# Kernel optimization log

Measured on AMD Instinct MI355X. Metric: run time of the kernel, lower is better.

Reference implementation:

```python
import jax, jax.numpy as jnp
import numpy as np

ANCHORS = np.array([[116.0, 90.0], [156.0, 198.0], [373.0, 326.0]], dtype=np.float32)
IMAGE_SIZE = 2048.0
IGNORE_THRES = 0.5
OBJ_SCALE = 100.0
NO_OBJ_SCALE = 1.0
EPS = 1e-16
BCE_EPS = 1e-12


def _wh_iou(anchors, gwh):
    # anchors: [A,2], gwh: [T,2] -> iou [A,T]
    aw, ah = anchors[:, 0:1], anchors[:, 1:2]            # [A,1]
    gw, gh = gwh[None, :, 0], gwh[None, :, 1]            # [1,T]
    inter = jnp.minimum(aw, gw) * jnp.minimum(ah, gh)
    union = aw * ah + gw * gh - inter
    return inter / (union + EPS)


def _bbox_iou_xywh(box1, box2):
    # boxes [T,4] in (cx, cy, w, h)
    b1x1, b1x2 = box1[:, 0] - box1[:, 2] / 2, box1[:, 0] + box1[:, 2] / 2
    b1y1, b1y2 = box1[:, 1] - box1[:, 3] / 2, box1[:, 1] + box1[:, 3] / 2
    b2x1, b2x2 = box2[:, 0] - box2[:, 2] / 2, box2[:, 0] + box2[:, 2] / 2
    b2y1, b2y2 = box2[:, 1] - box2[:, 3] / 2, box2[:, 1] + box2[:, 3] / 2
    iw = jnp.clip(jnp.minimum(b1x2, b2x2) - jnp.maximum(b1x1, b2x1), 0.0)
    ih = jnp.clip(jnp.minimum(b1y2, b2y2) - jnp.maximum(b1y1, b2y1), 0.0)
    inter = iw * ih
    a1 = (b1x2 - b1x1) * (b1y2 - b1y1)
    a2 = (b2x2 - b2x1) * (b2y2 - b2y1)
    return inter / (a1 + a2 - inter + EPS)


def _masked_mean(v, m):
    return jnp.sum(v * m) / jnp.maximum(jnp.sum(m), 1.0)


def setup_inputs() -> dict:
    key = jax.random.key(0)
    k1, k2, k3 = jax.random.split(key, 3)
    B, A, G, T = 32, 3, 256, 4096
    x = jax.random.normal(k1, (B, A * 5, G, G), jnp.float32) * 0.1
    tb = jax.random.randint(k2, (T, 1), 0, B).astype(jnp.float32)
    tcls = jnp.zeros((T, 1), jnp.float32)
    txywh = jax.random.uniform(k3, (T, 4), jnp.float32, 0.02, 0.98)
    targets = jnp.concatenate([tb, tcls, txywh], axis=1)
    return {"x": x, "targets": targets}


def reference(x, targets):
    B, G = x.shape[0], x.shape[2]
    A = ANCHORS.shape[0]
    stride = IMAGE_SIZE / G

    pred = x.reshape(B, A, 5, G, G).transpose(0, 1, 3, 4, 2)  # [B,A,G,G,5]
    cx = jax.nn.sigmoid(pred[..., 0])
    cy = jax.nn.sigmoid(pred[..., 1])
    w = pred[..., 2]
    h = pred[..., 3]
    pred_conf = jax.nn.sigmoid(pred[..., 4])

    grid_x = jnp.arange(G, dtype=jnp.float32).reshape(1, 1, 1, G)
    grid_y = jnp.arange(G, dtype=jnp.float32).reshape(1, 1, G, 1)
    anchors = jnp.asarray(ANCHORS) / stride                      # [A,2]
    aw = anchors[:, 0].reshape(1, A, 1, 1)
    ah = anchors[:, 1].reshape(1, A, 1, 1)

    pred_boxes = jnp.stack(
        [grid_x + cx, grid_y + cy, jnp.exp(w) * aw, jnp.exp(h) * ah], axis=-1
    )  # [B,A,G,G,4]
    output = jnp.concatenate(
        [pred_boxes.reshape(B, -1, 4) * stride, pred_conf.reshape(B, -1, 1)], axis=-1
    )

    # ---- build_targets (YOLOv3) ----
    tbox = targets[:, 2:6] * G                                   # [T,4] grid units
    gxy, gwh = tbox[:, :2], tbox[:, 2:]
    ious = _wh_iou(anchors, gwh)                                 # [A,T]
    best_n = jnp.argmax(ious, axis=0)                            # [T]
    b = targets[:, 0].astype(jnp.int32)
    gi = jnp.clip(jnp.floor(gxy[:, 0]), 0, G - 1).astype(jnp.int32)
    gj = jnp.clip(jnp.floor(gxy[:, 1]), 0, G - 1).astype(jnp.int32)

    zeros = jnp.zeros((B, A, G, G), jnp.float32)
    obj_mask = zeros.at[b, best_n, gj, gi].set(1.0)
    no_obj_mask = jnp.ones((B, A, G, G), jnp.float32).at[b, best_n, gj, gi].set(0.0)
    aidx = jnp.arange(A)
    keep = (ious.T <= IGNORE_THRES).astype(jnp.float32)          # [T,A]
    no_obj_mask = no_obj_mask.at[
        b[:, None], aidx[None, :], gj[:, None], gi[:, None]
    ].min(keep)

    tx = zeros.at[b, best_n, gj, gi].set(gxy[:, 0] - gi.astype(jnp.float32))
    ty = zeros.at[b, best_n, gj, gi].set(gxy[:, 1] - gj.astype(jnp.float32))
    tw = zeros.at[b, best_n, gj, gi].set(jnp.log(gwh[:, 0] / anchors[best_n, 0] + EPS))
    th = zeros.at[b, best_n, gj, gi].set(jnp.log(gwh[:, 1] / anchors[best_n, 1] + EPS))
    tconf = obj_mask

    pbt = pred_boxes[b, best_n, gj, gi]                          # [T,4]
    iou_scores = zeros.at[b, best_n, gj, gi].set(_bbox_iou_xywh(pbt, tbox))

    # ---- losses ----
    loss_x = _masked_mean((cx - tx) ** 2, obj_mask)
    loss_y = _masked_mean((cy - ty) ** 2, obj_mask)
    loss_w = _masked_mean((w - tw) ** 2, obj_mask)
    loss_h = _masked_mean((h - th) ** 2, obj_mask)
    loss_bbox = loss_x + loss_y + loss_w + loss_h
    bce = -(tconf * jnp.log(pred_conf + BCE_EPS)
            + (1.0 - tconf) * jnp.log(1.0 - pred_conf + BCE_EPS))
    loss_conf_obj = _masked_mean(bce, obj_mask)
    loss_conf_no_obj = _masked_mean(bce, no_obj_mask)
    loss_conf = OBJ_SCALE * loss_conf_obj + NO_OBJ_SCALE * loss_conf_no_obj
    loss_layer = loss_bbox + loss_conf

    # ---- metrics (side-effect scalars in torch; returned stop_gradient'd) ----
    conf50 = (pred_conf > 0.5).astype(jnp.float32)
    iou50 = (iou_scores > 0.5).astype(jnp.float32)
    iou75 = (iou_scores > 0.75).astype(jnp.float32)
    detected = conf50 * tconf
    conf_obj = _masked_mean(pred_conf, obj_mask)
    conf_no_obj = _masked_mean(pred_conf, no_obj_mask)
    precision = jnp.sum(iou50 * detected) / (jnp.sum(conf50) + EPS)
    recall50 = jnp.sum(iou50 * detected) / (jnp.sum(obj_mask) + EPS)
    recall75 = jnp.sum(iou75 * detected) / (jnp.sum(obj_mask) + EPS)
    metrics = jax.lax.stop_gradient(jnp.stack([
        loss_x, loss_y, loss_w, loss_h, loss_bbox, loss_conf, loss_layer,
        conf_obj, conf_no_obj, precision, recall50, recall75,
    ]))
    return output, loss_layer, metrics
```

## Files before the change

### kernel.cpp

```cpp
#include <hip/hip_runtime.h>
#include <cmath>

#define NA 3
#define HSIZE 8192
#define HMASK (HSIZE - 1)

typedef float v4f __attribute__((ext_vector_type(4)));


__device__ __forceinline__ float sigf(float v){ return 1.0f/(1.0f + expf(-v)); }
__device__ __forceinline__ float fast_sig(float v){
  return __builtin_amdgcn_rcpf(1.0f + __expf(-v));
}
__device__ __forceinline__ unsigned hslot(unsigned key){
  return (key * 2654435761u) >> 19;
}

__global__ __launch_bounds__(256) void k_zero(int* __restrict__ p, int n){
  int i = blockIdx.x*256 + threadIdx.x;
  if (i < n) p[i] = 0;
}

__global__ __launch_bounds__(256) void k_targets(
    const float* __restrict__ targets, int T, int G, float stride,
    int* __restrict__ ocell, int* __restrict__ keyarr,
    int* __restrict__ A_key, int* __restrict__ A_val,
    int* __restrict__ B_key, int* __restrict__ B_bits, int* __restrict__ B_maxt)
{
  int t = blockIdx.x*256 + threadIdx.x;
  if (t >= T) return;
  const float* tr = targets + (size_t)t*6;
  int b = (int)tr[0];
  float gx = tr[2]*(float)G, gy = tr[3]*(float)G, gw = tr[4]*(float)G, gh = tr[5]*(float)G;
  float aw[NA] = {116.0f/stride, 156.0f/stride, 373.0f/stride};
  float ah[NA] = { 90.0f/stride, 198.0f/stride, 326.0f/stride};
  float best_iou = -1.0f; int best = 0; int bits = 0;
  #pragma unroll
  for (int a = 0; a < NA; ++a){
    float inter = fminf(aw[a], gw) * fminf(ah[a], gh);
    float uni   = aw[a]*ah[a] + gw*gh - inter;
    float iou   = inter / (uni + 1e-16f);
    if (iou > best_iou){ best_iou = iou; best = a; }
    if (iou > 0.5f) bits |= (1 << a);
  }
  bits |= (1 << best);
  int gi = (int)floorf(gx); gi = gi < 0 ? 0 : (gi > G-1 ? G-1 : gi);
  int gj = (int)floorf(gy); gj = gj < 0 ? 0 : (gj > G-1 ? G-1 : gj);
  int cell = (b*G + gj)*G + gi;
  int okey = cell*4 + best;
  ocell[t]  = okey;
  keyarr[t] = (cell << 3) | bits;

  unsigned s = hslot((unsigned)okey) & HMASK;
  for (;;){
    int prev = atomicCAS(&A_key[s], 0, okey+1);
    if (prev == 0 || prev == okey+1){ atomicMax(&A_val[s], t+1); break; }
    s = (s+1) & HMASK;
  }
  s = hslot((unsigned)cell) & HMASK;
  for (;;){
    int prev = atomicCAS(&B_key[s], 0, cell+1);
    if (prev == 0 || prev == cell+1){
      atomicOr(&B_bits[s], bits);
      atomicMax(&B_maxt[s], t+1);
      break;
    }
    s = (s+1) & HMASK;
  }
}

__global__ __launch_bounds__(256, 7) void k_main(
    const float* __restrict__ x, const float* __restrict__ targets,
    float* __restrict__ out, double* __restrict__ sums,
    int T, int G, float stride, int total_cells, int nblkT,
    const int* __restrict__ ocell, const int* __restrict__ keyarr,
    const int* __restrict__ A_key, const int* __restrict__ A_val,
    const int* __restrict__ B_key, const int* __restrict__ B_bits,
    const int* __restrict__ B_maxt)
{
  int tid = threadIdx.x;

  if ((int)blockIdx.x < nblkT){
    int t = blockIdx.x*256 + tid;
    double v[12];
    #pragma unroll
    for (int k = 0; k < 12; ++k) v[k] = 0.0;

    if (t < T){
      const float* tr = targets + (size_t)t*6;
      int b = (int)tr[0];
      float gx = tr[2]*(float)G, gy = tr[3]*(float)G, gw = tr[4]*(float)G, gh = tr[5]*(float)G;
      int okey = ocell[t];
      int myk  = keyarr[t];
      int cell = myk >> 3;
      int best = okey & 3;
      int gi = cell % G;
      int gj = (cell / G) % G;
      int GG = G*G;

      unsigned s = hslot((unsigned)okey) & HMASK;
      while (A_key[s] != okey+1) s = (s+1) & HMASK;
      bool owner = (A_val[s] == t+1);

      if (owner){
        float awb = (best==0 ? 116.0f : (best==1 ? 156.0f : 373.0f)) / stride;
        float ahb = (best==0 ?  90.0f : (best==1 ? 198.0f : 326.0f)) / stride;
        const float* xp = x + ((size_t)(b*(NA*5) + best*5))*GG + (size_t)gj*G + gi;
        float x0 = xp[0], x1 = xp[(size_t)GG], x2 = xp[(size_t)2*GG],
              x3 = xp[(size_t)3*GG], x4 = xp[(size_t)4*GG];
        float cx = sigf(x0), cy = sigf(x1), w = x2, h = x3, conf = sigf(x4);
        float tx = gx - (float)gi, ty = gy - (float)gj;
        float tw = logf(gw/awb + 1e-16f), th = logf(gh/ahb + 1e-16f);
        v[3] = (double)((cx-tx)*(cx-tx));
        v[4] = (double)((cy-ty)*(cy-ty));
        v[5] = (double)((w-tw)*(w-tw));
        v[6] = (double)((h-th)*(h-th));
        v[7] = (double)(-logf(conf + 1e-12f));
        v[8] = (double)conf;
        float px = (float)gi + cx, py = (float)gj + cy;
        float pw = expf(w)*awb, ph = expf(h)*ahb;
        float iw = fminf(px + pw*0.5f, gx + gw*0.5f) - fmaxf(px - pw*0.5f, gx - gw*0.5f);
        float ih = fminf(py + ph*0.5f, gy + gh*0.5f) - fmaxf(py - ph*0.5f, gy - gh*0.5f);
        iw = fmaxf(iw, 0.0f); ih = fmaxf(ih, 0.0f);
        float inter = iw*ih;
        float iou = inter / (pw*ph + gw*gh - inter + 1e-16f);
        bool det = conf > 0.5f;
        v[9]  = (iou > 0.5f  && det) ? 1.0 : 0.0;
        v[10] = (iou > 0.75f && det) ? 1.0 : 0.0;
        v[11] = 1.0;
      }

      s = hslot((unsigned)cell) & HMASK;
      while (B_key[s] != cell+1) s = (s+1) & HMASK;
      if (B_maxt[s] == t+1){
        int bits = B_bits[s];
        #pragma unroll
        for (int a = 0; a < NA; ++a){
          if (bits & (1 << a)){
            float x4 = x[((size_t)(b*(NA*5) + a*5 + 4))*GG + (size_t)gj*G + gi];
            float conf = sigf(x4);
            v[0] += (double)(-logf(1.0f - conf + 1e-12f));
            v[1] += (double)conf;
            v[2] += 1.0;
          }
        }
      }
    }

    #pragma unroll
    for (int k = 0; k < 12; ++k){
      #pragma unroll
      for (int off = 32; off > 0; off >>= 1) v[k] += __shfl_down(v[k], off);
    }
    __shared__ double sred12[4][12];
    int lane = tid & 63, wv = tid >> 6;
    if (lane == 0){
      #pragma unroll
      for (int k = 0; k < 12; ++k) sred12[wv][k] = v[k];
    }
    __syncthreads();
    if (tid < 12){
      double sm = sred12[0][tid] + sred12[1][tid] + sred12[2][tid] + sred12[3][tid];
      unsafeAtomicAdd(&sums[3 + tid], sm);
    }
    return;
  }

  __shared__ float lds[256*21];
  int dblk = blockIdx.x - nblkT;
  int i = dblk*256 + tid;
  int cell = i*4;
  float nb = 0.0f, cs = 0.0f; int c50 = 0;

  if (cell < total_cells){
    int GG = G*G;
    int gx    = cell % G;
    int row   = cell / G;
    int gy    = row % G;
    int plane = row / G;
    int a     = plane % NA;
    float aw = (a==0 ? 116.0f : (a==1 ? 156.0f : 373.0f)) / stride;
    float ah = (a==0 ?  90.0f : (a==1 ? 198.0f : 326.0f)) / stride;

    size_t base = (size_t)plane*5*GG + (size_t)gy*G + gx;
    v4f p0 = *(const v4f*)(x + base);
    v4f p1 = *(const v4f*)(x + base + (size_t)GG);
    v4f p2 = *(const v4f*)(x + base + (size_t)2*GG);
    v4f p3 = *(const v4f*)(x + base + (size_t)3*GG);
    v4f p4 = *(const v4f*)(x + base + (size_t)4*GG);

    float* myl = lds + tid*21;
    #pragma unroll
    for (int j = 0; j < 4; ++j){
      float cx   = fast_sig(p0[j]);
      float cy   = fast_sig(p1[j]);
      float pw   = __expf(p2[j])*aw;
      float ph   = __expf(p3[j])*ah;
      float conf = fast_sig(p4[j]);
      myl[j*5+0] = ((float)(gx + j) + cx)*stride;
      myl[j*5+1] = ((float)gy + cy)*stride;
      myl[j*5+2] = pw*stride;
      myl[j*5+3] = ph*stride;
      myl[j*5+4] = conf;
      nb -= __logf(1.0f - conf + 1e-12f);
      cs += conf;
      c50 += (conf > 0.5f) ? 1 : 0;
    }
  }
  __syncthreads();

  int lane = tid & 63, wv = tid >> 6;
  {
    size_t waveBase = ((size_t)dblk*1024 + (size_t)(wv*256))*5;
    size_t totalF = (size_t)total_cells*5;
    const float* wl = lds + (size_t)(wv*64)*21;
    #pragma unroll
    for (int c = 0; c < 5; ++c){
      int f = (c*64 + lane)*4;
      if (waveBase + (size_t)f < totalF){
        int owner = f / 20;
        int within = f - owner*20;
        const float* src = wl + owner*21 + within;
        v4f val;
        val.x = src[0]; val.y = src[1]; val.z = src[2]; val.w = src[3];
        __builtin_nontemporal_store(val, (v4f*)(out + waveBase + f));
      }
    }
  }

  float vals[3] = {nb, cs, (float)c50};
  #pragma unroll
  for (int k = 0; k < 3; ++k){
    #pragma unroll
    for (int off = 32; off > 0; off >>= 1) vals[k] += __shfl_down(vals[k], off);
  }
  __shared__ double sred3[4][3];
  if (lane == 0){
    sred3[wv][0] = (double)vals[0];
    sred3[wv][1] = (double)vals[1];
    sred3[wv][2] = (double)vals[2];
  }
  __syncthreads();
  if (tid < 3){
    double sm = sred3[0][tid] + sred3[1][tid] + sred3[2][tid] + sred3[3][tid];
    unsafeAtomicAdd(&sums[tid], sm);
  }
}

__global__ __launch_bounds__(64) void k_final(
    const double* __restrict__ sums, float* __restrict__ tail, double total_cells)
{
  if (threadIdx.x != 0) return;
  double nb_all = sums[0], conf_all = sums[1], c50_all = sums[2];
  double enb = sums[3], econf = sums[4], ecnt = sums[5];
  double lx = sums[6], ly = sums[7], lw = sums[8], lh = sums[9];
  double bce = sums[10], cobj = sums[11], i50 = sums[12], i75 = sums[13], nobj = sums[14];

  double dObj = fmax(nobj, 1.0);
  double n_noobj = total_cells - ecnt;
  double dNo  = fmax(n_noobj, 1.0);

  double loss_x = lx/dObj, loss_y = ly/dObj, loss_w = lw/dObj, loss_h = lh/dObj;
  double loss_bbox = loss_x + loss_y + loss_w + loss_h;
  double loss_conf_obj   = bce/dObj;
  double loss_conf_noobj = (nb_all - enb)/dNo;
  double loss_conf  = 100.0*loss_conf_obj + 1.0*loss_conf_noobj;
  double loss_layer = loss_bbox + loss_conf;
  double conf_obj   = cobj/dObj;
  double conf_noobj = (conf_all - econf)/dNo;
  double precision  = i50/(c50_all + 1e-16);
  double recall50   = i50/(nobj + 1e-16);
  double recall75   = i75/(nobj + 1e-16);

  tail[0]  = (float)loss_layer;
  tail[1]  = (float)loss_x;
  tail[2]  = (float)loss_y;
  tail[3]  = (float)loss_w;
  tail[4]  = (float)loss_h;
  tail[5]  = (float)loss_bbox;
  tail[6]  = (float)loss_conf;
  tail[7]  = (float)loss_layer;
  tail[8]  = (float)conf_obj;
  tail[9]  = (float)conf_noobj;
  tail[10] = (float)precision;
  tail[11] = (float)recall50;
  tail[12] = (float)recall75;
}

extern "C" void kernel_launch(void* const* d_in, const int* in_sizes, int n_in,
                              void* d_out, int out_size, void* d_ws, size_t ws_size,
                              hipStream_t stream) {
  const float* x       = (const float*)d_in[0];
  const float* targets = (const float*)d_in[1];
  float* out = (float*)d_out;

  const int B = 32;
  int GG = in_sizes[0] / (B * NA * 5);
  int G = (int)(sqrt((double)GG) + 0.5);
  int T = in_sizes[1] / 6;
  float stride = 2048.0f / (float)G;

  char* ws = (char*)d_ws;
  double* sums  = (double*)ws;
  int* A_key  = (int*)(ws + 128);
  int* A_val  = A_key + HSIZE;
  int* B_key  = A_val + HSIZE;
  int* B_bits = B_key + HSIZE;
  int* B_maxt = B_bits + HSIZE;
  int* ocell  = B_maxt + HSIZE;
  int* keyarr = ocell + T;

  int total_cells = B * NA * GG;
  int nzero = 32 + 5*HSIZE;
  int nblkZ = (nzero + 255) / 256;
  int nblkT = (T + 255) / 256;
  int nblkD = (total_cells + 1023) / 1024;

  k_zero   <<<nblkZ, 256, 0, stream>>>((int*)ws, nzero);
  k_targets<<<nblkT, 256, 0, stream>>>(targets, T, G, stride, ocell, keyarr,
                                       A_key, A_val, B_key, B_bits, B_maxt);
  k_main   <<<nblkT + nblkD, 256, 0, stream>>>(x, targets, out, sums,
                                       T, G, stride, total_cells, nblkT,
                                       ocell, keyarr,
                                       A_key, A_val, B_key, B_bits, B_maxt);
  k_final  <<<1, 64, 0, stream>>>(sums, out + (size_t)total_cells*5, (double)total_cells);
}
```

Before: 259.4 us.

## Process eight cells per thread, drop LDS staging, fuse final kernel via ticket

```diff
diff --git a/kernel.cpp b/kernel.cpp
--- a/kernel.cpp
+++ b/kernel.cpp
@@ -69,16 +69,18 @@
   }
 }
 
-__global__ __launch_bounds__(256, 7) void k_main(
+__global__ __launch_bounds__(256) void k_main(
     const float* __restrict__ x, const float* __restrict__ targets,
-    float* __restrict__ out, double* __restrict__ sums,
-    int T, int G, float stride, int total_cells, int nblkT,
+    float* __restrict__ out, double* __restrict__ sums, int* __restrict__ ticket,
+    int T, int G, float stride, int total_cells, int nblkT, int nblkTot,
     const int* __restrict__ ocell, const int* __restrict__ keyarr,
     const int* __restrict__ A_key, const int* __restrict__ A_val,
     const int* __restrict__ B_key, const int* __restrict__ B_bits,
     const int* __restrict__ B_maxt)
 {
+  __shared__ double sred[4][12];
   int tid = threadIdx.x;
+  int lane = tid & 63, wv = tid >> 6;
 
   if ((int)blockIdx.x < nblkT){
     int t = blockIdx.x*256 + tid;
@@ -152,139 +154,132 @@
       #pragma unroll
       for (int off = 32; off > 0; off >>= 1) v[k] += __shfl_down(v[k], off);
     }
-    __shared__ double sred12[4][12];
-    int lane = tid & 63, wv = tid >> 6;
     if (lane == 0){
       #pragma unroll
-      for (int k = 0; k < 12; ++k) sred12[wv][k] = v[k];
+      for (int k = 0; k < 12; ++k) sred[wv][k] = v[k];
     }
     __syncthreads();
     if (tid < 12){
-      double sm = sred12[0][tid] + sred12[1][tid] + sred12[2][tid] + sred12[3][tid];
+      double sm = sred[0][tid] + sred[1][tid] + sred[2][tid] + sred[3][tid];
       unsafeAtomicAdd(&sums[3 + tid], sm);
     }
-    return;
-  }
-
-  __shared__ float lds[256*21];
-  int dblk = blockIdx.x - nblkT;
-  int i = dblk*256 + tid;
-  int cell = i*4;
-  float nb = 0.0f, cs = 0.0f; int c50 = 0;
-
-  if (cell < total_cells){
-    int GG = G*G;
-    int gx    = cell % G;
-    int row   = cell / G;
-    int gy    = row % G;
-    int plane = row / G;
-    int a     = plane % NA;
-    float aw = (a==0 ? 116.0f : (a==1 ? 156.0f : 373.0f)) / stride;
-    float ah = (a==0 ?  90.0f : (a==1 ? 198.0f : 326.0f)) / stride;
-
-    size_t base = (size_t)plane*5*GG + (size_t)gy*G + gx;
-    v4f p0 = *(const v4f*)(x + base);
-    v4f p1 = *(const v4f*)(x + base + (size_t)GG);
-    v4f p2 = *(const v4f*)(x + base + (size_t)2*GG);
-    v4f p3 = *(const v4f*)(x + base + (size_t)3*GG);
-    v4f p4 = *(const v4f*)(x + base + (size_t)4*GG);
-
-    float* myl = lds + tid*21;
+  } else {
+    int dblk = blockIdx.x - nblkT;
+    int i = dblk*256 + tid;
+    int cell = i*8;
+    float nb = 0.0f, cs = 0.0f; int c50 = 0;
+
+    if (cell < total_cells){
+      int GG = G*G;
+      int gx    = cell % G;
+      int row   = cell / G;
+      int gy    = row % G;
+      int plane = row / G;
+      int a     = plane % NA;
+      float aw = (a==0 ? 116.0f : (a==1 ? 156.0f : 373.0f)) / stride;
+      float ah = (a==0 ?  90.0f : (a==1 ? 198.0f : 326.0f)) / stride;
+
+      size_t base = (size_t)plane*5*GG + (size_t)gy*G + gx;
+      v4f p[5][2];
+      #pragma unroll
+      for (int c = 0; c < 5; ++c){
+        const v4f* pp = (const v4f*)(x + base + (size_t)c*GG);
+        p[c][0] = pp[0];
+        p[c][1] = pp[1];
+      }
+
+      float o[40];
+      #pragma unroll
+      for (int j = 0; j < 8; ++j){
+        float cx   = fast_sig(p[0][j>>2][j&3]);
+        float cy   = fast_sig(p[1][j>>2][j&3]);
+        float pw   = __expf(p[2][j>>2][j&3])*aw;
+        float ph   = __expf(p[3][j>>2][j&3])*ah;
+        float conf = fast_sig(p[4][j>>2][j&3]);
+        o[j*5+0] = ((float)(gx + j) + cx)*stride;
+        o[j*5+1] = ((float)gy + cy)*stride;
+        o[j*5+2] = pw*stride;
+        o[j*5+3] = ph*stride;
+        o[j*5+4] = conf;
+        nb -= __logf(1.0f - conf + 1e-12f);
+        cs += conf;
+        c50 += (conf > 0.5f) ? 1 : 0;
+      }
+
+      float* ob = out + (size_t)i*40;
+      #pragma unroll
+      for (int q = 0; q < 10; ++q){
+        v4f val = { o[q*4+0], o[q*4+1], o[q*4+2], o[q*4+3] };
+        __builtin_nontemporal_store(val, (v4f*)ob + q);
+      }
+    }
+
+    float vals[3] = {nb, cs, (float)c50};
     #pragma unroll
-    for (int j = 0; j < 4; ++j){
-      float cx   = fast_sig(p0[j]);
-      float cy   = fast_sig(p1[j]);
-      float pw   = __expf(p2[j])*aw;
-      float ph   = __expf(p3[j])*ah;
-      float conf = fast_sig(p4[j]);
-      myl[j*5+0] = ((float)(gx + j) + cx)*stride;
-      myl[j*5+1] = ((float)gy + cy)*stride;
-      myl[j*5+2] = pw*stride;
-      myl[j*5+3] = ph*stride;
-      myl[j*5+4] = conf;
-      nb -= __logf(1.0f - conf + 1e-12f);
-      cs += conf;
-      c50 += (conf > 0.5f) ? 1 : 0;
-    }
-  }
+    for (int k = 0; k < 3; ++k){
+      #pragma unroll
+      for (int off = 32; off > 0; off >>= 1) vals[k] += __shfl_down(vals[k], off);
+    }
+    if (lane == 0){
+      sred[wv][0] = (double)vals[0];
+      sred[wv][1] = (double)vals[1];
+      sred[wv][2] = (double)vals[2];
+    }
+    __syncthreads();
+    if (tid < 3){
+      double sm = sred[0][tid] + sred[1][tid] + sred[2][tid] + sred[3][tid];
+      unsafeAtomicAdd(&sums[tid], sm);
+    }
+  }
+
   __syncthreads();
-
-  int lane = tid & 63, wv = tid >> 6;
-  {
-    size_t waveBase = ((size_t)dblk*1024 + (size_t)(wv*256))*5;
-    size_t totalF = (size_t)total_cells*5;
-    const float* wl = lds + (size_t)(wv*64)*21;
-    #pragma unroll
-    for (int c = 0; c < 5; ++c){
-      int f = (c*64 + lane)*4;
-      if (waveBase + (size_t)f < totalF){
-        int owner = f / 20;
-        int within = f - owner*20;
-        const float* src = wl + owner*21 + within;
-        v4f val;
-        val.x = src[0]; val.y = src[1]; val.z = src[2]; val.w = src[3];
-        __builtin_nontemporal_store(val, (v4f*)(out + waveBase + f));
-      }
-    }
-  }
-
-  float vals[3] = {nb, cs, (float)c50};
-  #pragma unroll
-  for (int k = 0; k < 3; ++k){
-    #pragma unroll
-    for (int off = 32; off > 0; off >>= 1) vals[k] += __shfl_down(vals[k], off);
-  }
-  __shared__ double sred3[4][3];
-  if (lane == 0){
-    sred3[wv][0] = (double)vals[0];
-    sred3[wv][1] = (double)vals[1];
-    sred3[wv][2] = (double)vals[2];
-  }
-  __syncthreads();
-  if (tid < 3){
-    double sm = sred3[0][tid] + sred3[1][tid] + sred3[2][tid] + sred3[3][tid];
-    unsafeAtomicAdd(&sums[tid], sm);
-  }
-}
-
-__global__ __launch_bounds__(64) void k_final(
-    const double* __restrict__ sums, float* __restrict__ tail, double total_cells)
-{
-  if (threadIdx.x != 0) return;
-  double nb_all = sums[0], conf_all = sums[1], c50_all = sums[2];
-  double enb = sums[3], econf = sums[4], ecnt = sums[5];
-  double lx = sums[6], ly = sums[7], lw = sums[8], lh = sums[9];
-  double bce = sums[10], cobj = sums[11], i50 = sums[12], i75 = sums[13], nobj = sums[14];
-
-  double dObj = fmax(nobj, 1.0);
-  double n_noobj = total_cells - ecnt;
-  double dNo  = fmax(n_noobj, 1.0);
-
-  double loss_x = lx/dObj, loss_y = ly/dObj, loss_w = lw/dObj, loss_h = lh/dObj;
-  double loss_bbox = loss_x + loss_y + loss_w + loss_h;
-  double loss_conf_obj   = bce/dObj;
-  double loss_conf_noobj = (nb_all - enb)/dNo;
-  double loss_conf  = 100.0*loss_conf_obj + 1.0*loss_conf_noobj;
-  double loss_layer = loss_bbox + loss_conf;
-  double conf_obj   = cobj/dObj;
-  double conf_noobj = (conf_all - econf)/dNo;
-  double precision  = i50/(c50_all + 1e-16);
-  double recall50   = i50/(nobj + 1e-16);
-  double recall75   = i75/(nobj + 1e-16);
-
-  tail[0]  = (float)loss_layer;
-  tail[1]  = (float)loss_x;
-  tail[2]  = (float)loss_y;
-  tail[3]  = (float)loss_w;
-  tail[4]  = (float)loss_h;
-  tail[5]  = (float)loss_bbox;
-  tail[6]  = (float)loss_conf;
-  tail[7]  = (float)loss_layer;
-  tail[8]  = (float)conf_obj;
-  tail[9]  = (float)conf_noobj;
-  tail[10] = (float)precision;
-  tail[11] = (float)recall50;
-  tail[12] = (float)recall75;
+  if (tid == 0){
+    __threadfence();
+    int old = atomicAdd(ticket, 1);
+    if (old == nblkTot - 1){
+      __threadfence();
+      double s[15];
+      #pragma unroll
+      for (int k = 0; k < 15; ++k)
+        s[k] = __hip_atomic_load(&sums[k], __ATOMIC_RELAXED, __HIP_MEMORY_SCOPE_AGENT);
+      double nb_all = s[0], conf_all = s[1], c50_all = s[2];
+      double enb = s[3], econf = s[4], ecnt = s[5];
+      double lx = s[6], ly = s[7], lw = s[8], lh = s[9];
+      double bce = s[10], cobj = s[11], i50 = s[12], i75 = s[13], nobj = s[14];
+
+      double tc = (double)total_cells;
+      double dObj = fmax(nobj, 1.0);
+      double n_noobj = tc - ecnt;
+      double dNo  = fmax(n_noobj, 1.0);
+
+      double loss_x = lx/dObj, loss_y = ly/dObj, loss_w = lw/dObj, loss_h = lh/dObj;
+      double loss_bbox = loss_x + loss_y + loss_w + loss_h;
+      double loss_conf_obj   = bce/dObj;
+      double loss_conf_noobj = (nb_all - enb)/dNo;
+      double loss_conf  = 100.0*loss_conf_obj + 1.0*loss_conf_noobj;
+      double loss_layer = loss_bbox + loss_conf;
+      double conf_obj   = cobj/dObj;
+      double conf_noobj = (conf_all - econf)/dNo;
+      double precision  = i50/(c50_all + 1e-16);
+      double recall50   = i50/(nobj + 1e-16);
+      double recall75   = i75/(nobj + 1e-16);
+
+      float* tail = out + (size_t)total_cells*5;
+      tail[0]  = (float)loss_layer;
+      tail[1]  = (float)loss_x;
+      tail[2]  = (float)loss_y;
+      tail[3]  = (float)loss_w;
+      tail[4]  = (float)loss_h;
+      tail[5]  = (float)loss_bbox;
+      tail[6]  = (float)loss_conf;
+      tail[7]  = (float)loss_layer;
+      tail[8]  = (float)conf_obj;
+      tail[9]  = (float)conf_noobj;
+      tail[10] = (float)precision;
+      tail[11] = (float)recall50;
+      tail[12] = (float)recall75;
+    }
+  }
 }
 
 extern "C" void kernel_launch(void* const* d_in, const int* in_sizes, int n_in,
@@ -302,6 +297,7 @@
 
   char* ws = (char*)d_ws;
   double* sums  = (double*)ws;
+  int* ticket = (int*)(ws + 120);
   int* A_key  = (int*)(ws + 128);
   int* A_val  = A_key + HSIZE;
   int* B_key  = A_val + HSIZE;
@@ -314,14 +310,14 @@
   int nzero = 32 + 5*HSIZE;
   int nblkZ = (nzero + 255) / 256;
   int nblkT = (T + 255) / 256;
-  int nblkD = (total_cells + 1023) / 1024;
+  int nblkD = (total_cells + 2047) / 2048;
+  int nblkTot = nblkT + nblkD;
 
   k_zero   <<<nblkZ, 256, 0, stream>>>((int*)ws, nzero);
   k_targets<<<nblkT, 256, 0, stream>>>(targets, T, G, stride, ocell, keyarr,
                                        A_key, A_val, B_key, B_bits, B_maxt);
-  k_main   <<<nblkT + nblkD, 256, 0, stream>>>(x, targets, out, sums,
-                                       T, G, stride, total_cells, nblkT,
+  k_main   <<<nblkTot, 256, 0, stream>>>(x, targets, out, sums, ticket,
+                                       T, G, stride, total_cells, nblkT, nblkTot,
                                        ocell, keyarr,
                                        A_key, A_val, B_key, B_bits, B_maxt);
-  k_final  <<<1, 64, 0, stream>>>(sums, out + (size_t)total_cells*5, (double)total_cells);
-}
+}
```

Result: slower. 630.6 us (+143.1%).
